# Optimization experiments

Hardware: AMD Instinct MI355X
Metric: run time of the kernel (lower is better)

Reference implementation:

```python
import jax, jax.numpy as jnp
import numpy as np

INPUT_DIM = 4096
HIDDEN_DIMS = [2048, 1024, 512]
OUTPUT_DIM = 2
LAYER_DIMS = [INPUT_DIM] + HIDDEN_DIMS + [OUTPUT_DIM]
LAYER_IDX = np.concatenate([[0], np.cumsum(LAYER_DIMS)]).astype(int).tolist()
TOTAL_NODES = LAYER_IDX[-1]
FAN_IN = 128
BATCH = 512
EPS = 1e-5


def setup_inputs() -> dict:
    # Layered edge topology: each node in layer i receives FAN_IN random edges
    # from layer i-1 (matches how BINN uses set_connections).
    rng = np.random.default_rng(0)
    srcs, tgts = [], []
    for i in range(1, len(LAYER_DIMS)):
        ps, pe = LAYER_IDX[i - 1], LAYER_IDX[i]
        s, e = LAYER_IDX[i], LAYER_IDX[i + 1]
        dim = e - s
        srcs.append(rng.integers(ps, pe, size=(dim, FAN_IN)).reshape(-1))
        tgts.append(np.repeat(np.arange(s, e), FAN_IN))
    edge_src = jnp.asarray(np.concatenate(srcs), jnp.int32)
    edge_tgt = jnp.asarray(np.concatenate(tgts), jnp.int32)
    E = edge_src.shape[0]

    key = jax.random.key(0)
    kx, kw = jax.random.split(key)
    x = jax.random.normal(kx, (BATCH, INPUT_DIM), jnp.float32)
    # weight = randn(E) * 1/sqrt(fan_in)  (fan_in is FAN_IN for every target)
    weight = jax.random.normal(kw, (E,), jnp.float32) * (1.0 / np.sqrt(FAN_IN))
    bias = jnp.zeros((TOTAL_NODES - INPUT_DIM,), jnp.float32)
    n_hidden = sum(HIDDEN_DIMS)
    ln_gamma = jnp.ones((n_hidden,), jnp.float32)
    ln_beta = jnp.zeros((n_hidden,), jnp.float32)
    return dict(x=x, weight=weight, bias=bias, ln_gamma=ln_gamma,
                ln_beta=ln_beta, edge_src=edge_src, edge_tgt=edge_tgt)


def reference(x, weight, bias, ln_gamma, ln_beta, edge_src, edge_tgt):
    # activations held as [total_nodes, B] so segment_sum scatters on axis 0
    B = x.shape[0]
    acts = jnp.zeros((TOTAL_NODES, B), x.dtype).at[:INPUT_DIM].set(x.T)
    n_layers = len(LAYER_DIMS)
    for i in range(1, n_layers):  # fixed small layer count
        # full sparse mm over ALL edges each layer (faithful to original)
        contrib = weight[:, None] * acts[edge_src]            # [E, B]
        ws = jax.ops.segment_sum(contrib, edge_tgt,
                                 num_segments=TOTAL_NODES)    # [N, B]
        s, e = LAYER_IDX[i], LAYER_IDX[i + 1]
        cur = ws[s:e] + bias[s - INPUT_DIM:e - INPUT_DIM, None]
        if i < n_layers - 1:
            hs, he = s - INPUT_DIM, e - INPUT_DIM
            mean = jnp.mean(cur, axis=0, keepdims=True)
            var = jnp.var(cur, axis=0, keepdims=True)  # biased, as torch LN
            cur = (ln_gamma[hs:he, None] * (cur - mean) * jax.lax.rsqrt(var + EPS)
                   + ln_beta[hs:he, None])
            cur = jax.nn.relu(cur)
        acts = acts.at[s:e].set(cur)
    return acts[LAYER_IDX[-2]:LAYER_IDX[-1]].T  # [B, output_dim]
```

## Files before the change

### kernel.cpp

```cpp
#include <hip/hip_runtime.h>

#define BATCH 512
#define FAN_IN 128
#define EPS 1e-5f

typedef unsigned short u16;
typedef unsigned int u32;
typedef __attribute__((ext_vector_type(8))) short short8;
typedef __attribute__((ext_vector_type(4))) float f32x4;

__device__ __forceinline__ u16 f2bf(float f) {
    union { float f; u32 u; } v; v.f = f;
    u32 r = v.u + 0x7fffu + ((v.u >> 16) & 1u);
    return (u16)(r >> 16);
}
__device__ __forceinline__ void ld16(const void* g, void* l) {
    __builtin_amdgcn_global_load_lds(
        (const __attribute__((address_space(1))) u32*)g,
        (__attribute__((address_space(3))) u32*)l, 16, 0, 0);
}

__device__ __forceinline__ void densify_node(
    float* row, int Kin, int ebase, int srcbase, u16* outrow,
    const float* __restrict__ weight, const int* __restrict__ edge_src) {
    const int t = threadIdx.x;
    for (int k = t; k < Kin; k += 256) row[k] = 0.f;
    __syncthreads();
    if (t < FAN_IN)
        atomicAdd(&row[edge_src[ebase + t] - srcbase], weight[ebase + t]);
    __syncthreads();
    for (int k0 = t * 8; k0 < Kin; k0 += 2048) {
        u16 pk[8];
#pragma unroll
        for (int i = 0; i < 8; ++i) pk[i] = f2bf(row[k0 + i]);
        *(uint4*)(outrow + k0) = *(const uint4*)pk;
    }
}

__global__ __launch_bounds__(256) void prep(
    const float* __restrict__ weight, const int* __restrict__ edge_src,
    const float* __restrict__ x, u16* __restrict__ Wd, u16* __restrict__ xb) {
    __shared__ float row[4096];
    const int bid = blockIdx.x, t = threadIdx.x;
    if (bid < 2048) {
        densify_node(row, 4096, bid * 128, 0, Wd + (size_t)bid * 4096,
                     weight, edge_src);
    } else {
        const int b = bid - 2048;
        const float* xr = x + (size_t)b * 4096;
        u16* xo = xb + (size_t)b * 4096;
        for (int k0 = t * 8; k0 < 4096; k0 += 2048) {
            const float4 f0 = *(const float4*)(xr + k0);
            const float4 f1 = *(const float4*)(xr + k0 + 4);
            uint4 pk;
            pk.x = f2bf(f0.x) | ((u32)f2bf(f0.y) << 16);
            pk.y = f2bf(f0.z) | ((u32)f2bf(f0.w) << 16);
            pk.z = f2bf(f1.x) | ((u32)f2bf(f1.y) << 16);
            pk.w = f2bf(f1.z) | ((u32)f2bf(f1.w) << 16);
            *(uint4*)(xo + k0) = pk;
        }
    }
}

__device__ __forceinline__ void gemm_body(
    u16* SM, int m_t, int n_t, int z, const u16* __restrict__ Act,
    const u16* __restrict__ W, float* __restrict__ Cz, int M, int K,
    int kchunk) {
    u16* sA = SM;
    u16* sB = SM + 4096;
    const int tid = threadIdx.x;
    const int m0 = m_t * 64, n0 = n_t * 64, kbase = z * kchunk;
    float* Cp = Cz + (size_t)z * BATCH * M;

    const int r = tid >> 2, c = tid & 3;
    const int q = c ^ ((r ^ (r >> 2)) & 3);
    const u16* gA = Act + (size_t)(n0 + r) * K + kbase + q * 8;
    const u16* gB = W + (size_t)(m0 + r) * K + kbase + q * 8;
    const int lo = tid * 8;

    const int wave = tid >> 6, lane = tid & 63;
    const int l15 = lane & 15, quad = lane >> 4;
    const int aoff = (wave & 1) * 32, boff = (wave >> 1) * 32;
    int offA[2], offB[2];
#pragma unroll
    for (int i = 0; i < 2; ++i) {
        const int ra = aoff + i * 16 + l15;
        offA[i] = ra * 32 + ((quad ^ ((ra ^ (ra >> 2)) & 3)) * 8);
        const int rb = boff + i * 16 + l15;
        offB[i] = rb * 32 + ((quad ^ ((rb ^ (rb >> 2)) & 3)) * 8);
    }

    f32x4 acc[2][2] = {};
    const int niter = kchunk >> 5;
    ld16(gA, &sA[lo]); ld16(gB, &sB[lo]);
    for (int it = 0; it < niter; ++it) {
        __syncthreads();
        if (it + 1 < niter) {
            const int k0 = (it + 1) << 5;
            const int nb = ((it + 1) & 1) * 2048;
            ld16(gA + k0, &sA[nb + lo]); ld16(gB + k0, &sB[nb + lo]);
        }
        const u16* a = sA + (it & 1) * 2048;
        const u16* b = sB + (it & 1) * 2048;
        const short8 a0 = *(const short8*)(a + offA[0]);
        const short8 a1 = *(const short8*)(a + offA[1]);
        const short8 b0 = *(const short8*)(b + offB[0]);
        const short8 b1 = *(const short8*)(b + offB[1]);
        acc[0][0] = __builtin_amdgcn_mfma_f32_16x16x32_bf16(a0, b0, acc[0][0], 0, 0, 0);
        acc[0][1] = __builtin_amdgcn_mfma_f32_16x16x32_bf16(a0, b1, acc[0][1], 0, 0, 0);
        acc[1][0] = __builtin_amdgcn_mfma_f32_16x16x32_bf16(a1, b0, acc[1][0], 0, 0, 0);
        acc[1][1] = __builtin_amdgcn_mfma_f32_16x16x32_bf16(a1, b1, acc[1][1], 0, 0, 0);
    }
#pragma unroll
    for (int i = 0; i < 2; ++i) {
        const int nb = n_t * 64 + aoff + i * 16 + quad * 4;
#pragma unroll
        for (int rr = 0; rr < 4; ++rr)
#pragma unroll
            for (int j = 0; j < 2; ++j) {
                const int mg = m0 + boff + j * 16 + l15;
                Cp[(size_t)(nb + rr) * M + mg] = acc[i][j][rr];
            }
    }
}

__global__ __launch_bounds__(256, 8) void g1d(
    const u16* __restrict__ xb, u16* __restrict__ Wd, float* __restrict__ Cz1,
    const float* __restrict__ weight, const int* __restrict__ edge_src) {
    __shared__ u16 SM[8192];
    const int bid = blockIdx.x;
    if (bid < 1024) {
        gemm_body(SM, bid & 31, (bid >> 5) & 7, bid >> 8, xb, Wd, Cz1,
                  2048, 4096, 1024);
    } else if (bid < 2048) {
        const int u = bid - 1024;
        densify_node((float*)SM, 2048, 262144 + u * 128, 4096,
                     Wd + 8388608 + (size_t)u * 2048, weight, edge_src);
    } else {
        const int u = bid - 2048;
        densify_node((float*)SM, 1024, 393216 + u * 128, 6144,
                     Wd + 10485760 + (size_t)u * 1024, weight, edge_src);
    }
}

__global__ __launch_bounds__(256, 8) void gemm_bt(
    const u16* __restrict__ Act, const u16* __restrict__ W,
    float* __restrict__ Cz, int M, int K, int kchunk) {
    __shared__ u16 SM[8192];
    gemm_body(SM, blockIdx.x, blockIdx.y, blockIdx.z, Act, W, Cz, M, K, kchunk);
}

template <int M, int Z, bool WOUT>
__global__ __launch_bounds__(256) void fin(
    const float* __restrict__ Cz, const float* __restrict__ bias_l,
    const float* __restrict__ gamma_l, const float* __restrict__ beta_l,
    u16* __restrict__ actb, const float* __restrict__ weight,
    const int* __restrict__ edge_src, const float* __restrict__ obias,
    float* __restrict__ out) {
    __shared__ float rowL[M];
    __shared__ float red[8];
    __shared__ float mrs[2];
    __shared__ float w_s[256];
    __shared__ int   s_s[256];
    __shared__ float pr[256];

    const int n = blockIdx.x, t = threadIdx.x;
    const size_t zs = (size_t)BATCH * M;
    const float* base = Cz + (size_t)n * M;

    if (WOUT) { w_s[t] = weight[458752 + t]; s_s[t] = edge_src[458752 + t] - 7168; }

    float sum = 0.f, sq = 0.f;
    for (int m = t * 4; m < M; m += 1024) {
        float4 v = *(const float4*)(bias_l + m);
#pragma unroll
        for (int z = 0; z < Z; ++z) {
            const float4 cv = *(const float4*)(base + (size_t)z * zs + m);
            v.x += cv.x; v.y += cv.y; v.z += cv.z; v.w += cv.w;
        }
        *(float4*)(rowL + m) = v;
        sum += v.x + v.y + v.z + v.w;
        sq += v.x * v.x + v.y * v.y + v.z * v.z + v.w * v.w;
    }
#pragma unroll
    for (int o = 32; o; o >>= 1) { sum += __shfl_down(sum, o); sq += __shfl_down(sq, o); }
    if ((t & 63) == 0) { red[(t >> 6) * 2] = sum; red[(t >> 6) * 2 + 1] = sq; }
    __syncthreads();
    if (t == 0) {
        const float s = red[0] + red[2] + red[4] + red[6];
        const float qq = red[1] + red[3] + red[5] + red[7];
        const float mean = s / (float)M;
        const float var = qq / (float)M - mean * mean;
        mrs[0] = mean; mrs[1] = rsqrtf(var + EPS);
    }
    __syncthreads();
    const float mean = mrs[0], rstd = mrs[1];

    for (int m = t * 4; m < M; m += 1024) {
        const float4 v = *(const float4*)(rowL + m);
        const float4 g = *(const float4*)(gamma_l + m);
        const float4 bt = *(const float4*)(beta_l + m);
        const float o0 = fmaxf(fmaf(g.x * (v.x - mean), rstd, bt.x), 0.f);
        const float o1 = fmaxf(fmaf(g.y * (v.y - mean), rstd, bt.y), 0.f);
        const float o2 = fmaxf(fmaf(g.z * (v.z - mean), rstd, bt.z), 0.f);
        const float o3 = fmaxf(fmaf(g.w * (v.w - mean), rstd, bt.w), 0.f);
        if (WOUT) {
            rowL[m + 0] = o0; rowL[m + 1] = o1; rowL[m + 2] = o2; rowL[m + 3] = o3;
        } else {
            u16 pk[4] = {f2bf(o0), f2bf(o1), f2bf(o2), f2bf(o3)};
            *(uint2*)(actb + (size_t)n * M + m) = *(const uint2*)pk;
        }
    }
    if (WOUT) {
        __syncthreads();
        pr[t] = w_s[t] * rowL[s_s[t]];
        __syncthreads();
        if (t < 2) {
            float s = 0.f;
            for (int k = 0; k < FAN_IN; ++k) s += pr[t * FAN_IN + k];
            out[(size_t)n * 2 + t] = s + obias[t];
        }
    }
}

extern "C" void kernel_launch(void* const* d_in, const int* in_sizes, int n_in,
                              void* d_out, int out_size, void* d_ws, size_t ws_size,
                              hipStream_t stream) {
    const float* x        = (const float*)d_in[0];
    const float* weight   = (const float*)d_in[1];
    const float* bias     = (const float*)d_in[2];
    const float* ln_gamma = (const float*)d_in[3];
    const float* ln_beta  = (const float*)d_in[4];
    const int*   edge_src = (const int*)d_in[5];
    float* out = (float*)d_out;

    float* Cz1 = (float*)d_ws;
    float* Cz2 = Cz1 + (size_t)4 * 512 * 2048;
    float* Cz3 = Cz2 + (size_t)4 * 512 * 1024;
    u16* xb    = (u16*)(Cz3 + (size_t)8 * 512 * 512);
    u16* actb1 = xb + (size_t)512 * 4096;
    u16* actb2 = actb1 + (size_t)512 * 2048;
    u16* Wd    = actb2 + (size_t)512 * 1024;

    prep<<<2560, 256, 0, stream>>>(weight, edge_src, x, Wd, xb);
    g1d<<<2560, 256, 0, stream>>>(xb, Wd, Cz1, weight, edge_src);
    fin<2048, 4, false><<<512, 256, 0, stream>>>(
        Cz1, bias, ln_gamma, ln_beta, actb1, nullptr, nullptr, nullptr, nullptr);
    gemm_bt<<<dim3(16, 8, 4), 256, 0, stream>>>(actb1, Wd + 8388608, Cz2,
                                                1024, 2048, 512);
    fin<1024, 4, false><<<512, 256, 0, stream>>>(
        Cz2, bias + 2048, ln_gamma + 2048, ln_beta + 2048, actb2,
        nullptr, nullptr, nullptr, nullptr);
    gemm_bt<<<dim3(8, 8, 8), 256, 0, stream>>>(actb2, Wd + 10485760, Cz3,
                                               512, 1024, 128);
    fin<512, 8, true><<<512, 256, 0, stream>>>(
        Cz3, bias + 3072, ln_gamma + 3072, ln_beta + 3072, nullptr,
        weight, edge_src, bias + 3584, out);
}
```

Before: 124.0 us.

## Use 128x128 tiled GEMM with 8-way split-K for first layer

Adds a new GEMM body with 128x128 output tiles per block, where each wave computes a 64x64 sub-tile with 4x4 MFMA accumulators, double-buffered LDS and swizzled layout. The first-layer GEMM now uses it with 512 blocks and an 8-way K split instead of 1024 smaller 64-tile blocks with a 4-way split. The finalize kernel for that layer now sums 8 partial slices. The aim is more reuse per LDS load and fewer global loads, at the cost of higher register pressure (lower occupancy, since the launch-bound occupancy hint is dropped), twice as much partial-sum traffic, and a larger workspace.

```diff
diff --git a/kernel.cpp b/kernel.cpp
--- a/kernel.cpp
+++ b/kernel.cpp
@@ -124,20 +124,91 @@
     }
 }
 
-__global__ __launch_bounds__(256, 8) void g1d(
+__device__ __forceinline__ void gemm128_body(
+    u16* SM, int m_t, int n_t, int z, const u16* __restrict__ Act,
+    const u16* __restrict__ W, float* __restrict__ Cz, int M, int K,
+    int kchunk) {
+    u16* sA = SM;
+    u16* sB = SM + 8192;
+    const int tid = threadIdx.x;
+    const int m0 = m_t * 128, n0 = n_t * 128, kbase = z * kchunk;
+    float* Cp = Cz + (size_t)z * BATCH * M;
+
+    const int r = tid >> 2, c = tid & 3;
+    const int q1 = c ^ ((r ^ (r >> 2)) & 3);
+    const int r2 = r + 64;
+    const int q2 = c ^ ((r2 ^ (r2 >> 2)) & 3);
+    const u16* gA1 = Act + (size_t)(n0 + r) * K + kbase + q1 * 8;
+    const u16* gA2 = Act + (size_t)(n0 + r2) * K + kbase + q2 * 8;
+    const u16* gB1 = W + (size_t)(m0 + r) * K + kbase + q1 * 8;
+    const u16* gB2 = W + (size_t)(m0 + r2) * K + kbase + q2 * 8;
+    const int lo1 = tid * 8, lo2 = tid * 8 + 2048;
+
+    const int wave = tid >> 6, lane = tid & 63;
+    const int l15 = lane & 15, quad = lane >> 4;
+    const int wn = (wave & 1) * 64, wm = (wave >> 1) * 64;
+    int offA[4], offB[4];
+#pragma unroll
+    for (int i = 0; i < 4; ++i) {
+        const int na = wn + i * 16 + l15;
+        offA[i] = na * 32 + ((quad ^ ((na ^ (na >> 2)) & 3)) * 8);
+        const int mb = wm + i * 16 + l15;
+        offB[i] = mb * 32 + ((quad ^ ((mb ^ (mb >> 2)) & 3)) * 8);
+    }
+
+    f32x4 acc[4][4] = {};
+    const int niter = kchunk >> 5;
+    ld16(gA1, &sA[lo1]); ld16(gA2, &sA[lo2]);
+    ld16(gB1, &sB[lo1]); ld16(gB2, &sB[lo2]);
+    for (int it = 0; it < niter; ++it) {
+        __syncthreads();
+        if (it + 1 < niter) {
+            const int k0 = (it + 1) << 5;
+            const int nb = ((it + 1) & 1) * 4096;
+            ld16(gA1 + k0, &sA[nb + lo1]); ld16(gA2 + k0, &sA[nb + lo2]);
+            ld16(gB1 + k0, &sB[nb + lo1]); ld16(gB2 + k0, &sB[nb + lo2]);
+        }
+        const u16* a = sA + (it & 1) * 4096;
+        const u16* b = sB + (it & 1) * 4096;
+        short8 av[4], bv[4];
+#pragma unroll
+        for (int i = 0; i < 4; ++i) av[i] = *(const short8*)(a + offA[i]);
+#pragma unroll
+        for (int j = 0; j < 4; ++j) bv[j] = *(const short8*)(b + offB[j]);
+#pragma unroll
+        for (int i = 0; i < 4; ++i)
+#pragma unroll
+            for (int j = 0; j < 4; ++j)
+                acc[i][j] = __builtin_amdgcn_mfma_f32_16x16x32_bf16(
+                    av[i], bv[j], acc[i][j], 0, 0, 0);
+    }
+#pragma unroll
+    for (int i = 0; i < 4; ++i) {
+        const int nb = n0 + wn + i * 16 + quad * 4;
+#pragma unroll
+        for (int rr = 0; rr < 4; ++rr)
+#pragma unroll
+            for (int j = 0; j < 4; ++j) {
+                const int mg = m0 + wm + j * 16 + l15;
+                Cp[(size_t)(nb + rr) * M + mg] = acc[i][j][rr];
+            }
+    }
+}
+
+__global__ __launch_bounds__(256) void g1d(
     const u16* __restrict__ xb, u16* __restrict__ Wd, float* __restrict__ Cz1,
     const float* __restrict__ weight, const int* __restrict__ edge_src) {
-    __shared__ u16 SM[8192];
+    __shared__ u16 SM[16384];
     const int bid = blockIdx.x;
-    if (bid < 1024) {
-        gemm_body(SM, bid & 31, (bid >> 5) & 7, bid >> 8, xb, Wd, Cz1,
-                  2048, 4096, 1024);
-    } else if (bid < 2048) {
-        const int u = bid - 1024;
+    if (bid < 512) {
+        gemm128_body(SM, bid & 15, (bid >> 4) & 3, bid >> 6, xb, Wd, Cz1,
+                     2048, 4096, 512);
+    } else if (bid < 1536) {
+        const int u = bid - 512;
         densify_node((float*)SM, 2048, 262144 + u * 128, 4096,
                      Wd + 8388608 + (size_t)u * 2048, weight, edge_src);
     } else {
-        const int u = bid - 2048;
+        const int u = bid - 1536;
         densify_node((float*)SM, 1024, 393216 + u * 128, 6144,
                      Wd + 10485760 + (size_t)u * 1024, weight, edge_src);
     }
@@ -235,7 +306,7 @@
     float* out = (float*)d_out;
 
     float* Cz1 = (float*)d_ws;
-    float* Cz2 = Cz1 + (size_t)4 * 512 * 2048;
+    float* Cz2 = Cz1 + (size_t)8 * 512 * 2048;
     float* Cz3 = Cz2 + (size_t)4 * 512 * 1024;
     u16* xb    = (u16*)(Cz3 + (size_t)8 * 512 * 512);
     u16* actb1 = xb + (size_t)512 * 4096;
@@ -243,8 +314,8 @@
     u16* Wd    = actb2 + (size_t)512 * 1024;
 
     prep<<<2560, 256, 0, stream>>>(weight, edge_src, x, Wd, xb);
-    g1d<<<2560, 256, 0, stream>>>(xb, Wd, Cz1, weight, edge_src);
-    fin<2048, 4, false><<<512, 256, 0, stream>>>(
+    g1d<<<2048, 256, 0, stream>>>(xb, Wd, Cz1, weight, edge_src);
+    fin<2048, 8, false><<<512, 256, 0, stream>>>(
         Cz1, bias, ln_gamma, ln_beta, actb1, nullptr, nullptr, nullptr, nullptr);
     gemm_bt<<<dim3(16, 8, 4), 256, 0, stream>>>(actb1, Wd + 8388608, Cz2,
                                                 1024, 2048, 512);
```

Result: faster. 121.2 us (-2.2%).
